# Performance work log

Measured on AMD Instinct MI355X. Metric: run time of the kernel, lower is better.

## Reference

```python
import jax, jax.numpy as jnp
import numpy as np

N_NODES = 100000
N_EDGES = 3200000
N_GRAPHS = 64


def _seg_mean(vals, idx, num_segments):
    s = jax.ops.segment_sum(vals, idx, num_segments=num_segments)
    cnt = jax.ops.segment_sum(jnp.ones((vals.shape[0],), vals.dtype), idx,
                              num_segments=num_segments)
    return s / jnp.maximum(cnt, 1.0)[:, None]


def _gcn_layer(x, edge_index, edge_attr, Wc, bc, Wn):
    # center = lin1(x)
    center = x @ Wc + bc
    row, col = edge_index[0], edge_index[1]  # row = source (j), col = target (i)
    # degree computed over row indices (as in PyG degree(row))
    deg = jax.ops.segment_sum(jnp.ones((row.shape[0],), x.dtype), row,
                              num_segments=x.shape[0])
    deg_inv_sqrt = jnp.where(deg > 0, jax.lax.rsqrt(jnp.maximum(deg, 1.0)), 0.0)
    norm = deg_inv_sqrt[row] * deg_inv_sqrt[col]  # [E]
    # message: lin2(concat(x_j, edge_attr)) * norm
    msg = jnp.concatenate([x[row], edge_attr], axis=1) @ Wn  # [E, out]
    msg = msg * norm[:, None]
    # aggr='mean' at target nodes
    aggr = _seg_mean(msg, col, x.shape[0])
    return center + aggr


def setup_inputs() -> dict:
    key = jax.random.key(0)
    ks = jax.random.split(key, 12)
    x = jax.random.normal(ks[0], (N_NODES, 3), dtype=jnp.float32)
    edge_index = jax.random.randint(ks[1], (2, N_EDGES), 0, N_NODES, dtype=jnp.int64)
    edge_attr = jax.random.normal(ks[2], (N_EDGES, 2), dtype=jnp.float32)
    batch = jnp.sort(jax.random.randint(ks[3], (N_NODES,), 0, N_GRAPHS, dtype=jnp.int64))
    s = 0.2
    params = {
        'Wc1': jax.random.normal(ks[4], (3, 16), jnp.float32) * s,
        'bc1': jnp.zeros((16,), jnp.float32),
        'Wn1': jax.random.normal(ks[5], (5, 16), jnp.float32) * s,   # in+edge = 3+2
        'Wc2': jax.random.normal(ks[6], (16, 16), jnp.float32) * s,
        'bc2': jnp.zeros((16,), jnp.float32),
        'Wn2': jax.random.normal(ks[7], (18, 16), jnp.float32) * s,  # 16+2
        'Wl1': jax.random.normal(ks[8], (16, 16), jnp.float32) * s,
        'bl1': jnp.zeros((16,), jnp.float32),
        'Wl2': jax.random.normal(ks[9], (16, 2), jnp.float32) * s,
        'bl2': jnp.zeros((2,), jnp.float32),
    }
    return dict(x=x, edge_index=edge_index, edge_attr=edge_attr, batch=batch, **params)


def reference(x, edge_index, edge_attr, batch,
              Wc1, bc1, Wn1, Wc2, bc2, Wn2, Wl1, bl1, Wl2, bl2):
    h = _gcn_layer(x, edge_index, edge_attr, Wc1, bc1, Wn1)
    h = jax.nn.relu(h)  # dropout is identity in eval mode
    h = _gcn_layer(h, edge_index, edge_attr, Wc2, bc2, Wn2)
    h = jax.nn.relu(h)
    g = _seg_mean(h, batch, N_GRAPHS)          # global scatter_mean pooling [G,16]
    g = jax.nn.relu(g @ Wl1 + bl1)
    return g @ Wl2 + bl2                        # [G, 2]
```

## Files before the change

kernel.cpp:

```cpp
#include <hip/hip_runtime.h>

constexpr int TPB  = 256;
constexpr int TPBW = 1024;
constexpr int TPBS = 512;
constexpr int BSH  = 7;
constexpr int BKN  = 128;
constexpr int MAXB = 800;
constexpr int CAP  = 4608;
constexpr int SBUF = 4608;
constexpr int ITER = 9;
constexpr int SIT  = 7;
constexpr int SEDG = SIT * TPBW;
constexpr int HWL  = 12800;

__device__ __forceinline__ unsigned short f2bf(float f) {
    unsigned u = __float_as_uint(f);
    u += 0x7FFFu + ((u >> 16) & 1u);
    return (unsigned short)(u >> 16);
}
__device__ __forceinline__ float bflo(unsigned u) {
    return __uint_as_float(u << 16);
}
__device__ __forceinline__ float bfhi(unsigned u) {
    return __uint_as_float(u & 0xFFFF0000u);
}

__global__ __launch_bounds__(TPBW)
void k_stage2(const int* __restrict__ ei, const float2* __restrict__ ea,
              int E, int NBKT, int W,
              int* __restrict__ gcnt, int2* __restrict__ staged,
              unsigned int* __restrict__ partialR) {
    __shared__ unsigned int lh[HWL];
    __shared__ int2 sb2[SEDG];
    __shared__ unsigned short sbk[SEDG];
    __shared__ int cl[MAXB], gb[MAXB], rs[MAXB + 1];
    __shared__ int tmp[1024];
    const int p = blockIdx.x, t = threadIdx.x;
    for (int i = t; i < W; i += TPBW) lh[i] = 0;
    for (int b = t; b < NBKT; b += TPBW) cl[b] = 0;
    __syncthreads();
    const int* colA = ei + E;
    const int s = p * SEDG, send = min(s + SEDG, E);
    int rid[SIT], eap[SIT], bk[SIT], rk[SIT];
#pragma unroll
    for (int k = 0; k < SIT; k++) {
        int e = s + t + k * TPBW;
        bk[k] = -1;
        if (e < send) {
            int r = ei[e], c = colA[e];
            atomicAdd(&lh[r >> 3], 1u << ((r & 7) * 4));
            int b = c >> BSH;
            float2 ev = ea[e];
            rid[k] = (r << BSH) | (c & (BKN - 1));
            eap[k] = (int)((unsigned)f2bf(ev.x) | ((unsigned)f2bf(ev.y) << 16));
            bk[k] = b;
            rk[k] = atomicAdd(&cl[b], 1);
        }
    }
    __syncthreads();
    tmp[t] = (t < NBKT) ? cl[t] : 0;
    __syncthreads();
    for (int off = 1; off < 1024; off <<= 1) {
        int add = (t >= off) ? tmp[t - off] : 0;
        __syncthreads();
        tmp[t] += add;
        __syncthreads();
    }
    if (t < NBKT) rs[t] = tmp[t] - cl[t];
    if (t == NBKT - 1) rs[NBKT] = tmp[t];
    __syncthreads();
    for (int b = t; b < NBKT; b += TPBW) {
        int c = cl[b];
        gb[b] = c ? atomicAdd(&gcnt[b], c) : 0;
    }
    __syncthreads();
#pragma unroll
    for (int k = 0; k < SIT; k++)
        if (bk[k] >= 0) {
            int slot = rs[bk[k]] + rk[k];
            sb2[slot] = make_int2(rid[k], eap[k]);
            sbk[slot] = (unsigned short)bk[k];
        }
    __syncthreads();
    const int total = rs[NBKT];
    for (int i = t; i < total; i += TPBW) {
        int b = sbk[i];
        int pos = gb[b] + (i - rs[b]);
        if (pos < CAP) staged[(size_t)b * CAP + pos] = sb2[i];
    }
    for (int w = t; w < W; w += TPBW) partialR[(size_t)p * W + w] = lh[w];
}

__global__ __launch_bounds__(512)
void k_xd(const unsigned int* __restrict__ partialR, int NP, int W, int N,
          const float* __restrict__ x,
          float* __restrict__ dis, float4* __restrict__ xd) {
    __shared__ unsigned int sA[8][64], sB[8][64];
    const int wloc = threadIdx.x & 63, lane = threadIdx.x >> 6;
    const int w = blockIdx.x * 64 + wloc;
    unsigned int accA = 0, accB = 0;
    if (w < W) {
        for (int p = lane; p < NP; p += 8) {
            unsigned int v = partialR[(size_t)p * W + w];
            accA += v & 0x0F0F0F0Fu;
            accB += (v >> 4) & 0x0F0F0F0Fu;
        }
    }
    sA[lane][wloc] = accA;
    sB[lane][wloc] = accB;
    __syncthreads();
    if (lane == 0 && w < W) {
#pragma unroll
        for (int l = 1; l < 8; l++) { accA += sA[l][wloc]; accB += sB[l][wloc]; }
        int d[8];
        d[0] = accA & 255; d[2] = (accA >> 8) & 255;
        d[4] = (accA >> 16) & 255; d[6] = accA >> 24;
        d[1] = accB & 255; d[3] = (accB >> 8) & 255;
        d[5] = (accB >> 16) & 255; d[7] = accB >> 24;
        const int n0 = w * 8;
#pragma unroll
        for (int k = 0; k < 8; k++) {
            int n = n0 + k;
            if (n < N) {
                float dv = d[k] ? rsqrtf((float)d[k]) : 0.f;
                dis[n] = dv;
                xd[n] = make_float4(x[3 * (size_t)n], x[3 * (size_t)n + 1],
                                    x[3 * (size_t)n + 2], dv);
            }
        }
    }
}

__global__ __launch_bounds__(TPBS)
void k_sortA(int2* __restrict__ staged, const int* __restrict__ gcnt,
             const float4* __restrict__ xd, int N,
             const float* __restrict__ Wc, const float* __restrict__ bc,
             const float* __restrict__ Wn,
             unsigned short* __restrict__ hb, unsigned short* __restrict__ hbs,
             float2* __restrict__ eaS,
             int* __restrict__ cnt, int* __restrict__ base, int* __restrict__ segN) {
    __shared__ int2 sbuf2[SBUF];
    __shared__ int lfill[BKN], lexc[BKN];
    __shared__ float sax[BKN], say[BKN], saz[BKN], se1[BKN], se2[BKN];
    __shared__ float sWc[48], sbc[16], sWn[80];
    __shared__ int stot;
    const int b = blockIdx.x, t = threadIdx.x;
    const size_t s0 = (size_t)b * CAP;
    const int c0 = b << BSH;
    int cb = gcnt[b]; if (cb > CAP) cb = CAP;
    if (t < BKN) lfill[t] = 0;
    if (t < 48) sWc[t] = Wc[t];
    if (t >= 64 && t < 80) sbc[t - 64] = bc[t - 64];
    if (t >= 128 && t < 208) sWn[t - 128] = Wn[t - 128];
    __syncthreads();
    int er[ITER], ep[ITER], rk[ITER];
#pragma unroll
    for (int k = 0; k < ITER; k++) {
        int e = t + k * TPBS;
        rk[k] = -1;
        if (e < cb) {
            int2 v = staged[s0 + e];
            int j = v.x & (BKN - 1);
            er[k] = (int)(((unsigned)v.x) >> BSH);
            ep[k] = v.y;
            rk[k] = atomicAdd(&lfill[j], 1) | (j << 16);
        }
    }
    __syncthreads();
    if (t < 64) {
        int v0 = lfill[2 * t], v1 = lfill[2 * t + 1];
        int sv = v0 + v1, incl = sv;
#pragma unroll
        for (int off = 1; off < 64; off <<= 1) {
            int up = __shfl_up(incl, off, 64);
            if (t >= off) incl += up;
        }
        int exc = incl - sv;
        lexc[2 * t]     = exc;
        lexc[2 * t + 1] = exc + v0;
        if (t == 63) stot = incl;
    }
    __syncthreads();
#pragma unroll
    for (int k = 0; k < ITER; k++) {
        if (rk[k] >= 0) {
            int j = rk[k] >> 16, rr = rk[k] & 0xFFFF;
            sbuf2[lexc[j] + rr] = make_int2(er[k], ep[k]);
        }
    }
    __syncthreads();
    int tot = stot; if (tot > SBUF) tot = SBUF;
    const int grp = t >> 2, sub = t & 3;
    const int node = c0 + grp;
    float a0 = 0.f, a1 = 0.f, a2 = 0.f, b1 = 0.f, b2 = 0.f;
    {
        int e0 = lexc[grp], dg = lfill[grp];
        if (node < N) {
            for (int e = sub; e < dg; e += 8) {
                int2 ve0 = sbuf2[e0 + e];
                bool v1 = (e + 4) < dg;
                int2 ve1 = v1 ? sbuf2[e0 + e + 4] : ve0;
                float4 q0 = xd[ve0.x];
                float4 q1 = xd[ve1.x];
                float w0 = q0.w;
                float w1 = v1 ? q1.w : 0.f;
                a0 += w0 * q0.x + w1 * q1.x;
                a1 += w0 * q0.y + w1 * q1.y;
                a2 += w0 * q0.z + w1 * q1.z;
                b1 += w0 * bflo((unsigned)ve0.y) + w1 * bflo((unsigned)ve1.y);
                b2 += w0 * bfhi((unsigned)ve0.y) + w1 * bfhi((unsigned)ve1.y);
            }
        }
    }
    a0 += __shfl_down(a0, 2, 4); a0 += __shfl_down(a0, 1, 4);
    a1 += __shfl_down(a1, 2, 4); a1 += __shfl_down(a1, 1, 4);
    a2 += __shfl_down(a2, 2, 4); a2 += __shfl_down(a2, 1, 4);
    b1 += __shfl_down(b1, 2, 4); b1 += __shfl_down(b1, 1, 4);
    b2 += __shfl_down(b2, 2, 4); b2 += __shfl_down(b2, 1, 4);
    if (sub == 0) {
        sax[grp] = a0; say[grp] = a1; saz[grp] = a2;
        se1[grp] = b1; se2[grp] = b2;
    }
    {
        int* ridS = (int*)staged;
        for (int i = t; i < tot; i += TPBS) ridS[s0 * 2 + i] = sbuf2[i].x;
    }
    if (t == 0) segN[b] = tot;
    if (t < BKN) {
        int nd = c0 + t;
        if (nd < N) { cnt[nd] = lfill[t]; base[nd] = lexc[t]; }
    }
    __syncthreads();
    if (t < BKN) {
        int nd = c0 + t;
        if (nd < N) {
            float inv = 1.0f / fmaxf((float)lfill[t], 1.0f);
            float4 xq = xd[nd];
            float ldt = xq.w;
            float sc = ldt * inv;
            float m[5] = {sax[t] * sc, say[t] * sc, saz[t] * sc,
                          se1[t] * sc, se2[t] * sc};
            float xv[3] = {xq.x, xq.y, xq.z};
            float o[16];
#pragma unroll
            for (int k = 0; k < 16; k++) {
                float v = sbc[k];
#pragma unroll
                for (int j = 0; j < 3; j++) v += xv[j] * sWc[j * 16 + k];
#pragma unroll
                for (int j = 0; j < 5; j++) v += m[j] * sWn[j * 16 + k];
                o[k] = fmaxf(v, 0.0f);
            }
            unsigned ov[8], sv[8];
#pragma unroll
            for (int q = 0; q < 8; q++) {
                ov[q] = (unsigned)f2bf(o[2 * q]) | ((unsigned)f2bf(o[2 * q + 1]) << 16);
                sv[q] = (unsigned)f2bf(ldt * o[2 * q]) |
                        ((unsigned)f2bf(ldt * o[2 * q + 1]) << 16);
            }
            uint4* hp = (uint4*)(hb + 16 * (size_t)nd);
            hp[0] = make_uint4(ov[0], ov[1], ov[2], ov[3]);
            hp[1] = make_uint4(ov[4], ov[5], ov[6], ov[7]);
            uint4* hps = (uint4*)(hbs + 16 * (size_t)nd);
            hps[0] = make_uint4(sv[0], sv[1], sv[2], sv[3]);
            hps[1] = make_uint4(sv[4], sv[5], sv[6], sv[7]);
            eaS[nd] = make_float2(se1[t] * ldt, se2[t] * ldt);
        }
    }
}

__global__ __launch_bounds__(TPBS)
void k_g2(const int* __restrict__ ridS, const int* __restrict__ cnt,
          const int* __restrict__ base, const int* __restrict__ segN,
          const float* __restrict__ dis, const unsigned short* __restrict__ hb,
          const unsigned short* __restrict__ hbs,
          const float2* __restrict__ eaS, const int* __restrict__ batch, int N,
          const float* __restrict__ Wc, const float* __restrict__ bc,
          const float* __restrict__ Wn,
          float* __restrict__ pool, int* __restrict__ poolcnt) {
    __shared__ int sbuf[SBUF];
    __shared__ int lfill[BKN], lexc[BKN];
    __shared__ float smr[BKN][17];
    __shared__ float sWc[256], sbc[16], sWn[288], sp[1024];
    __shared__ int sc[64];
    const int b = blockIdx.x, t = threadIdx.x;
    const size_t s0 = (size_t)b * CAP * 2;
    const int c0 = b << BSH;
    if (t < BKN) {
        int nd = c0 + t;
        lfill[t] = (nd < N) ? cnt[nd] : 0;
        lexc[t]  = (nd < N) ? base[nd] : 0;
    }
    for (int k = t; k < 256; k += TPBS) sWc[k] = Wc[k];
    for (int k = t; k < 16;  k += TPBS) sbc[k] = bc[k];
    for (int k = t; k < 288; k += TPBS) sWn[k] = Wn[k];
    for (int k = t; k < 1024; k += TPBS) sp[k] = 0.f;
    if (t < 64) sc[t] = 0;
    int tot = segN[b];
    if (tot > SBUF) tot = SBUF;
    for (int i = t; i < tot; i += TPBS) sbuf[i] = ridS[s0 + i];
    __syncthreads();
    const int grp = t >> 2, sub = t & 3;
    const int node = c0 + grp;
    float mm[16];
#pragma unroll
    for (int k = 0; k < 16; k++) mm[k] = 0.f;
    if (node < N) {
        int e0 = lexc[grp], dg = lfill[grp];
        for (int e = sub; e < dg; e += 8) {
            int r0 = sbuf[e0 + e];
            bool v1 = (e + 4) < dg;
            int r1 = v1 ? sbuf[e0 + e + 4] : r0;
            const uint4* h0 = (const uint4*)(hbs + 16 * (size_t)r0);
            const uint4* h1 = (const uint4*)(hbs + 16 * (size_t)r1);
            uint4 A0 = h0[0], B0 = h0[1];
            uint4 A1 = h1[0], B1 = h1[1];
            float s1 = v1 ? 1.f : 0.f;
            mm[0]  += bflo(A0.x) + s1 * bflo(A1.x);
            mm[1]  += bfhi(A0.x) + s1 * bfhi(A1.x);
            mm[2]  += bflo(A0.y) + s1 * bflo(A1.y);
            mm[3]  += bfhi(A0.y) + s1 * bfhi(A1.y);
            mm[4]  += bflo(A0.z) + s1 * bflo(A1.z);
            mm[5]  += bfhi(A0.z) + s1 * bfhi(A1.z);
            mm[6]  += bflo(A0.w) + s1 * bflo(A1.w);
            mm[7]  += bfhi(A0.w) + s1 * bfhi(A1.w);
            mm[8]  += bflo(B0.x) + s1 * bflo(B1.x);
            mm[9]  += bfhi(B0.x) + s1 * bfhi(B1.x);
            mm[10] += bflo(B0.y) + s1 * bflo(B1.y);
            mm[11] += bfhi(B0.y) + s1 * bfhi(B1.y);
            mm[12] += bflo(B0.z) + s1 * bflo(B1.z);
            mm[13] += bfhi(B0.z) + s1 * bfhi(B1.z);
            mm[14] += bflo(B0.w) + s1 * bflo(B1.w);
            mm[15] += bfhi(B0.w) + s1 * bfhi(B1.w);
        }
    }
#pragma unroll
    for (int k = 0; k < 16; k++) {
        mm[k] += __shfl_down(mm[k], 2, 4);
        mm[k] += __shfl_down(mm[k], 1, 4);
    }
    if (sub == 0) {
#pragma unroll
        for (int k = 0; k < 16; k++) smr[grp][k] = mm[k];
    }
    __syncthreads();
    if (t < BKN) {
        int nd = c0 + t;
        if (nd < N) {
            float inv = 1.0f / fmaxf((float)lfill[t], 1.0f);
            float ldt = dis[nd];
            float scm = ldt * inv;
            float m[18];
#pragma unroll
            for (int k = 0; k < 16; k++) m[k] = smr[t][k] * scm;
            float2 es = eaS[nd];
            m[16] = es.x * inv; m[17] = es.y * inv;
            const uint4* hp = (const uint4*)(hb + 16 * (size_t)nd);
            uint4 A = hp[0], B = hp[1];
            float hv[16] = {bflo(A.x), bfhi(A.x), bflo(A.y), bfhi(A.y),
                            bflo(A.z), bfhi(A.z), bflo(A.w), bfhi(A.w),
                            bflo(B.x), bfhi(B.x), bflo(B.y), bfhi(B.y),
                            bflo(B.z), bfhi(B.z), bflo(B.w), bfhi(B.w)};
            int g = batch[nd];
            atomicAdd(&sc[g], 1);
#pragma unroll
            for (int k = 0; k < 16; k++) {
                float v = sbc[k];
#pragma unroll
                for (int j = 0; j < 16; j++) v += hv[j] * sWc[j * 16 + k];
#pragma unroll
                for (int j = 0; j < 18; j++) v += m[j] * sWn[j * 16 + k];
                v = fmaxf(v, 0.0f);
                unsafeAtomicAdd(&sp[g * 16 + k], v);
            }
        }
    }
    __syncthreads();
    for (int k = t; k < 1024; k += TPBS)
        if (sp[k] != 0.0f) unsafeAtomicAdd(&pool[k], sp[k]);
    if (t < 64 && sc[t]) atomicAdd(&poolcnt[t], sc[t]);
}

__global__ void k_final(const float* __restrict__ pool, const int* __restrict__ poolcnt,
                        const float* __restrict__ Wl1, const float* __restrict__ bl1,
                        const float* __restrict__ Wl2, const float* __restrict__ bl2,
                        float* __restrict__ out) {
    int g = threadIdx.x;
    if (g >= 64) return;
    float inv = 1.0f / fmaxf((float)poolcnt[g], 1.0f);
    float gv[16];
#pragma unroll
    for (int k = 0; k < 16; k++) gv[k] = pool[g * 16 + k] * inv;
    float t[16];
#pragma unroll
    for (int k = 0; k < 16; k++) {
        float v = bl1[k];
#pragma unroll
        for (int j = 0; j < 16; j++) v += gv[j] * Wl1[j * 16 + k];
        t[k] = fmaxf(v, 0.0f);
    }
    float o0 = bl2[0], o1 = bl2[1];
#pragma unroll
    for (int j = 0; j < 16; j++) {
        o0 += t[j] * Wl2[j * 2 + 0];
        o1 += t[j] * Wl2[j * 2 + 1];
    }
    out[2 * g + 0] = o0;
    out[2 * g + 1] = o1;
}

extern "C" void kernel_launch(void* const* d_in, const int* in_sizes, int n_in,
                              void* d_out, int out_size, void* d_ws, size_t ws_size,
                              hipStream_t stream) {
    const float* x     = (const float*)d_in[0];
    const int*   ei    = (const int*)  d_in[1];
    const float* ea    = (const float*)d_in[2];
    const int*   batch = (const int*)  d_in[3];
    const float* Wc1   = (const float*)d_in[4];
    const float* bc1   = (const float*)d_in[5];
    const float* Wn1   = (const float*)d_in[6];
    const float* Wc2   = (const float*)d_in[7];
    const float* bc2   = (const float*)d_in[8];
    const float* Wn2   = (const float*)d_in[9];
    const float* Wl1   = (const float*)d_in[10];
    const float* bl1   = (const float*)d_in[11];
    const float* Wl2   = (const float*)d_in[12];
    const float* bl2   = (const float*)d_in[13];
    float* out = (float*)d_out;

    const int N  = in_sizes[0] / 3;
    const int E  = in_sizes[1] / 2;
    const int NBKT = (N + BKN - 1) >> BSH;
    const int SGRID = (E + SEDG - 1) / SEDG;
    const int W = (N + 7) >> 3;

    char* ws = (char*)d_ws;
    size_t o = 0;
    auto alloc = [&](size_t bytes) {
        void* p = ws + o;
        o += (bytes + 255) & ~(size_t)255;
        return p;
    };
    float* pool    = (float*)alloc(64 * 16 * 4);
    int*   poolcnt = (int*)  alloc(64 * 4);
    int*   gcnt    = (int*)  alloc((size_t)NBKT * 4);
    size_t zbytes = o;
    float*  dis     = (float*)alloc((size_t)N * 4);
    float4* xd      = (float4*)alloc((size_t)N * 16);
    float2* eaS     = (float2*)alloc((size_t)N * 8);
    int*    cnt     = (int*)  alloc((size_t)N * 4);
    int*    base    = (int*)  alloc((size_t)N * 4);
    int*    segN    = (int*)  alloc((size_t)NBKT * 4);
    unsigned int* partialR = (unsigned int*)alloc((size_t)SGRID * W * 4);
    int2*   staged  = (int2*)alloc((size_t)NBKT * CAP * 8);
    unsigned short* hb  = (unsigned short*)alloc((size_t)N * 16 * 2);
    unsigned short* hbs = (unsigned short*)alloc((size_t)N * 16 * 2);
    (void)ws_size;

    hipMemsetAsync(d_ws, 0, zbytes, stream);

    k_stage2<<<SGRID, TPBW, 0, stream>>>(ei, (const float2*)ea, E, NBKT, W,
                                         gcnt, staged, partialR);
    k_xd    <<<(W + 63) / 64, 512, 0, stream>>>(partialR, SGRID, W, N, x, dis, xd);
    k_sortA <<<NBKT, TPBS, 0, stream>>>(staged, gcnt, xd, N,
                                        Wc1, bc1, Wn1, hb, hbs, eaS,
                                        cnt, base, segN);
    k_g2    <<<NBKT, TPBS, 0, stream>>>((const int*)staged, cnt, base, segN,
                                        dis, hb, hbs, eaS, batch, N,
                                        Wc2, bc2, Wn2, pool, poolcnt);
    k_final <<<1, 64, 0, stream>>>(pool, poolcnt, Wl1, bl1, Wl2, bl2, out);
}
```

Before: 237.6 us.

## Fuse degree, layer1, layer2 and head into one cooperative persistent kernel

```diff
diff --git a/kernel.cpp b/kernel.cpp
--- a/kernel.cpp
+++ b/kernel.cpp
@@ -1,13 +1,14 @@
 #include <hip/hip_runtime.h>
-
-constexpr int TPB  = 256;
+#include <hip/hip_cooperative_groups.h>
+
+namespace cg = cooperative_groups;
+
 constexpr int TPBW = 1024;
 constexpr int TPBS = 512;
 constexpr int BSH  = 7;
 constexpr int BKN  = 128;
 constexpr int MAXB = 800;
-constexpr int CAP  = 4608;
-constexpr int SBUF = 4608;
+constexpr int CAP  = 4544;
 constexpr int ITER = 9;
 constexpr int SIT  = 7;
 constexpr int SEDG = SIT * TPBW;
@@ -91,322 +92,369 @@
     for (int w = t; w < W; w += TPBW) partialR[(size_t)p * W + w] = lh[w];
 }
 
-__global__ __launch_bounds__(512)
-void k_xd(const unsigned int* __restrict__ partialR, int NP, int W, int N,
-          const float* __restrict__ x,
-          float* __restrict__ dis, float4* __restrict__ xd) {
-    __shared__ unsigned int sA[8][64], sB[8][64];
-    const int wloc = threadIdx.x & 63, lane = threadIdx.x >> 6;
-    const int w = blockIdx.x * 64 + wloc;
-    unsigned int accA = 0, accB = 0;
-    if (w < W) {
-        for (int p = lane; p < NP; p += 8) {
-            unsigned int v = partialR[(size_t)p * W + w];
-            accA += v & 0x0F0F0F0Fu;
-            accB += (v >> 4) & 0x0F0F0F0Fu;
-        }
-    }
-    sA[lane][wloc] = accA;
-    sB[lane][wloc] = accB;
-    __syncthreads();
-    if (lane == 0 && w < W) {
-#pragma unroll
-        for (int l = 1; l < 8; l++) { accA += sA[l][wloc]; accB += sB[l][wloc]; }
-        int d[8];
-        d[0] = accA & 255; d[2] = (accA >> 8) & 255;
-        d[4] = (accA >> 16) & 255; d[6] = accA >> 24;
-        d[1] = accB & 255; d[3] = (accB >> 8) & 255;
-        d[5] = (accB >> 16) & 255; d[7] = accB >> 24;
-        const int n0 = w * 8;
-#pragma unroll
-        for (int k = 0; k < 8; k++) {
-            int n = n0 + k;
-            if (n < N) {
-                float dv = d[k] ? rsqrtf((float)d[k]) : 0.f;
-                dis[n] = dv;
-                xd[n] = make_float4(x[3 * (size_t)n], x[3 * (size_t)n + 1],
-                                    x[3 * (size_t)n + 2], dv);
-            }
-        }
-    }
-}
-
 __global__ __launch_bounds__(TPBS)
-void k_sortA(int2* __restrict__ staged, const int* __restrict__ gcnt,
-             const float4* __restrict__ xd, int N,
-             const float* __restrict__ Wc, const float* __restrict__ bc,
-             const float* __restrict__ Wn,
+void k_fused(int2* __restrict__ staged, const int* __restrict__ gcnt,
+             const unsigned int* __restrict__ partialR, int NP, int W, int N,
+             const float* __restrict__ x, float* __restrict__ dis,
+             float4* __restrict__ xd,
+             const float* __restrict__ Wc1, const float* __restrict__ bc1,
+             const float* __restrict__ Wn1,
              unsigned short* __restrict__ hb, unsigned short* __restrict__ hbs,
              float2* __restrict__ eaS,
-             int* __restrict__ cnt, int* __restrict__ base, int* __restrict__ segN) {
-    __shared__ int2 sbuf2[SBUF];
+             int* __restrict__ cnt, int* __restrict__ base, int* __restrict__ segN,
+             const int* __restrict__ batch,
+             const float* __restrict__ Wc2, const float* __restrict__ bc2,
+             const float* __restrict__ Wn2,
+             float* __restrict__ pool, int* __restrict__ poolcnt,
+             const float* __restrict__ Wl1, const float* __restrict__ bl1,
+             const float* __restrict__ Wl2, const float* __restrict__ bl2,
+             float* __restrict__ out, int NBKT) {
+    cg::grid_group grid = cg::this_grid();
+    __shared__ int2 sbuf2[CAP];
     __shared__ int lfill[BKN], lexc[BKN];
-    __shared__ float sax[BKN], say[BKN], saz[BKN], se1[BKN], se2[BKN];
-    __shared__ float sWc[48], sbc[16], sWn[80];
-    __shared__ int stot;
-    const int b = blockIdx.x, t = threadIdx.x;
-    const size_t s0 = (size_t)b * CAP;
-    const int c0 = b << BSH;
-    int cb = gcnt[b]; if (cb > CAP) cb = CAP;
-    if (t < BKN) lfill[t] = 0;
-    if (t < 48) sWc[t] = Wc[t];
-    if (t >= 64 && t < 80) sbc[t - 64] = bc[t - 64];
-    if (t >= 128 && t < 208) sWn[t - 128] = Wn[t - 128];
-    __syncthreads();
-    int er[ITER], ep[ITER], rk[ITER];
-#pragma unroll
-    for (int k = 0; k < ITER; k++) {
-        int e = t + k * TPBS;
-        rk[k] = -1;
-        if (e < cb) {
-            int2 v = staged[s0 + e];
-            int j = v.x & (BKN - 1);
-            er[k] = (int)(((unsigned)v.x) >> BSH);
-            ep[k] = v.y;
-            rk[k] = atomicAdd(&lfill[j], 1) | (j << 16);
-        }
-    }
-    __syncthreads();
-    if (t < 64) {
-        int v0 = lfill[2 * t], v1 = lfill[2 * t + 1];
-        int sv = v0 + v1, incl = sv;
-#pragma unroll
-        for (int off = 1; off < 64; off <<= 1) {
-            int up = __shfl_up(incl, off, 64);
-            if (t >= off) incl += up;
-        }
-        int exc = incl - sv;
-        lexc[2 * t]     = exc;
-        lexc[2 * t + 1] = exc + v0;
-        if (t == 63) stot = incl;
-    }
-    __syncthreads();
-#pragma unroll
-    for (int k = 0; k < ITER; k++) {
-        if (rk[k] >= 0) {
-            int j = rk[k] >> 16, rr = rk[k] & 0xFFFF;
-            sbuf2[lexc[j] + rr] = make_int2(er[k], ep[k]);
-        }
-    }
-    __syncthreads();
-    int tot = stot; if (tot > SBUF) tot = SBUF;
-    const int grp = t >> 2, sub = t & 3;
-    const int node = c0 + grp;
-    float a0 = 0.f, a1 = 0.f, a2 = 0.f, b1 = 0.f, b2 = 0.f;
+    __shared__ float facc[5][BKN];
+    __shared__ float sw1[144];
+    __shared__ int stot, keepTot;
+    int* ibuf = (int*)sbuf2;
+    const int t = threadIdx.x;
+
     {
-        int e0 = lexc[grp], dg = lfill[grp];
-        if (node < N) {
-            for (int e = sub; e < dg; e += 8) {
-                int2 ve0 = sbuf2[e0 + e];
-                bool v1 = (e + 4) < dg;
-                int2 ve1 = v1 ? sbuf2[e0 + e + 4] : ve0;
-                float4 q0 = xd[ve0.x];
-                float4 q1 = xd[ve1.x];
-                float w0 = q0.w;
-                float w1 = v1 ? q1.w : 0.f;
-                a0 += w0 * q0.x + w1 * q1.x;
-                a1 += w0 * q0.y + w1 * q1.y;
-                a2 += w0 * q0.z + w1 * q1.z;
-                b1 += w0 * bflo((unsigned)ve0.y) + w1 * bflo((unsigned)ve1.y);
-                b2 += w0 * bfhi((unsigned)ve0.y) + w1 * bfhi((unsigned)ve1.y);
-            }
-        }
-    }
-    a0 += __shfl_down(a0, 2, 4); a0 += __shfl_down(a0, 1, 4);
-    a1 += __shfl_down(a1, 2, 4); a1 += __shfl_down(a1, 1, 4);
-    a2 += __shfl_down(a2, 2, 4); a2 += __shfl_down(a2, 1, 4);
-    b1 += __shfl_down(b1, 2, 4); b1 += __shfl_down(b1, 1, 4);
-    b2 += __shfl_down(b2, 2, 4); b2 += __shfl_down(b2, 1, 4);
-    if (sub == 0) {
-        sax[grp] = a0; say[grp] = a1; saz[grp] = a2;
-        se1[grp] = b1; se2[grp] = b2;
-    }
-    {
-        int* ridS = (int*)staged;
-        for (int i = t; i < tot; i += TPBS) ridS[s0 * 2 + i] = sbuf2[i].x;
-    }
-    if (t == 0) segN[b] = tot;
-    if (t < BKN) {
-        int nd = c0 + t;
-        if (nd < N) { cnt[nd] = lfill[t]; base[nd] = lexc[t]; }
-    }
-    __syncthreads();
-    if (t < BKN) {
-        int nd = c0 + t;
-        if (nd < N) {
-            float inv = 1.0f / fmaxf((float)lfill[t], 1.0f);
-            float4 xq = xd[nd];
-            float ldt = xq.w;
-            float sc = ldt * inv;
-            float m[5] = {sax[t] * sc, say[t] * sc, saz[t] * sc,
-                          se1[t] * sc, se2[t] * sc};
-            float xv[3] = {xq.x, xq.y, xq.z};
-            float o[16];
+        const int nxb = (W + 63) >> 6;
+        if ((int)blockIdx.x < nxb) {
+            unsigned int* sA = (unsigned int*)ibuf;
+            unsigned int* sB = sA + 512;
+            const int wloc = t & 63, lane = t >> 6;
+            const int w = blockIdx.x * 64 + wloc;
+            unsigned int accA = 0, accB = 0;
+            if (w < W) {
+                for (int p = lane; p < NP; p += 8) {
+                    unsigned int v = partialR[(size_t)p * W + w];
+                    accA += v & 0x0F0F0F0Fu;
+                    accB += (v >> 4) & 0x0F0F0F0Fu;
+                }
+            }
+            sA[lane * 64 + wloc] = accA;
+            sB[lane * 64 + wloc] = accB;
+            __syncthreads();
+            if (lane == 0 && w < W) {
+#pragma unroll
+                for (int l = 1; l < 8; l++) {
+                    accA += sA[l * 64 + wloc];
+                    accB += sB[l * 64 + wloc];
+                }
+                int d[8];
+                d[0] = accA & 255; d[2] = (accA >> 8) & 255;
+                d[4] = (accA >> 16) & 255; d[6] = accA >> 24;
+                d[1] = accB & 255; d[3] = (accB >> 8) & 255;
+                d[5] = (accB >> 16) & 255; d[7] = accB >> 24;
+                const int n0 = w * 8;
+#pragma unroll
+                for (int k = 0; k < 8; k++) {
+                    int n = n0 + k;
+                    if (n < N) {
+                        float dv = d[k] ? rsqrtf((float)d[k]) : 0.f;
+                        dis[n] = dv;
+                        xd[n] = make_float4(x[3 * (size_t)n], x[3 * (size_t)n + 1],
+                                            x[3 * (size_t)n + 2], dv);
+                    }
+                }
+            }
+        }
+    }
+    __threadfence();
+    grid.sync();
+
+    if (t < 48) sw1[t] = Wc1[t];
+    else if (t < 64) sw1[t] = bc1[t - 48];
+    else if (t < 144) sw1[t] = Wn1[t - 64];
+
+    int own[4], nb = 0;
+    for (int b = blockIdx.x; b < NBKT && nb < 4; b += (int)gridDim.x) own[nb++] = b;
+
+    for (int q = 0; q < nb; q++) {
+        const int b = own[q];
+        const size_t s0 = (size_t)b * CAP;
+        const int c0 = b << BSH;
+        int cb = gcnt[b]; if (cb > CAP) cb = CAP;
+        __syncthreads();
+        if (t < BKN) {
+            lfill[t] = 0;
+            facc[0][t] = 0.f; facc[1][t] = 0.f; facc[2][t] = 0.f;
+            facc[3][t] = 0.f; facc[4][t] = 0.f;
+        }
+        __syncthreads();
+        int er[ITER], ep[ITER], rk[ITER];
+#pragma unroll
+        for (int k = 0; k < ITER; k++) {
+            int e = t + k * TPBS;
+            rk[k] = -1;
+            if (e < cb) {
+                int2 v = staged[s0 + e];
+                int j = v.x & (BKN - 1);
+                er[k] = (int)(((unsigned)v.x) >> BSH);
+                ep[k] = v.y;
+                rk[k] = atomicAdd(&lfill[j], 1) | (j << 16);
+            }
+        }
+        __syncthreads();
+        if (t < 64) {
+            int v0 = lfill[2 * t], v1 = lfill[2 * t + 1];
+            int sv = v0 + v1, incl = sv;
+#pragma unroll
+            for (int off = 1; off < 64; off <<= 1) {
+                int up = __shfl_up(incl, off, 64);
+                if (t >= off) incl += up;
+            }
+            int exc = incl - sv;
+            lexc[2 * t] = exc;
+            lexc[2 * t + 1] = exc + v0;
+            if (t == 63) stot = incl;
+        }
+        __syncthreads();
+#pragma unroll
+        for (int k = 0; k < ITER; k++) {
+            if (rk[k] >= 0) {
+                int j = rk[k] >> 16, rr = rk[k] & 0xFFFF;
+                sbuf2[lexc[j] + rr] = make_int2(er[k], ep[k]);
+            }
+        }
+        __syncthreads();
+        int tot = stot; if (tot > CAP) tot = CAP;
+        {
+            const int grp = t >> 2, sub = t & 3;
+            const int node = c0 + grp;
+            float a0 = 0.f, a1 = 0.f, a2 = 0.f, e1 = 0.f, e2 = 0.f;
+            int e0 = lexc[grp], dg = lfill[grp];
+            if (node < N) {
+                for (int e = sub; e < dg; e += 8) {
+                    int2 ve0 = sbuf2[e0 + e];
+                    bool ok1 = (e + 4) < dg;
+                    int2 ve1 = ok1 ? sbuf2[e0 + e + 4] : ve0;
+                    float4 q0 = xd[ve0.x];
+                    float4 q1 = xd[ve1.x];
+                    float w0 = q0.w;
+                    float w1v = ok1 ? q1.w : 0.f;
+                    a0 += w0 * q0.x + w1v * q1.x;
+                    a1 += w0 * q0.y + w1v * q1.y;
+                    a2 += w0 * q0.z + w1v * q1.z;
+                    e1 += w0 * bflo((unsigned)ve0.y) + w1v * bflo((unsigned)ve1.y);
+                    e2 += w0 * bfhi((unsigned)ve0.y) + w1v * bfhi((unsigned)ve1.y);
+                }
+            }
+            a0 += __shfl_down(a0, 2, 4); a0 += __shfl_down(a0, 1, 4);
+            a1 += __shfl_down(a1, 2, 4); a1 += __shfl_down(a1, 1, 4);
+            a2 += __shfl_down(a2, 2, 4); a2 += __shfl_down(a2, 1, 4);
+            e1 += __shfl_down(e1, 2, 4); e1 += __shfl_down(e1, 1, 4);
+            e2 += __shfl_down(e2, 2, 4); e2 += __shfl_down(e2, 1, 4);
+            if (sub == 0) {
+                facc[0][grp] = a0; facc[1][grp] = a1; facc[2][grp] = a2;
+                facc[3][grp] = e1; facc[4][grp] = e2;
+            }
+        }
+        if (t == 0) segN[b] = tot;
+        if (t < BKN) {
+            int nd = c0 + t;
+            if (nd < N) { cnt[nd] = lfill[t]; base[nd] = lexc[t]; }
+        }
+        __syncthreads();
+        if (q == nb - 1) {
+            int rv[ITER];
+#pragma unroll
+            for (int k = 0; k < ITER; k++) {
+                int i = t + k * TPBS;
+                rv[k] = (i < tot) ? sbuf2[i].x : 0;
+            }
+            __syncthreads();
+#pragma unroll
+            for (int k = 0; k < ITER; k++) {
+                int i = t + k * TPBS;
+                if (i < tot) ibuf[i] = rv[k];
+            }
+            if (t == 0) keepTot = tot;
+        } else {
+            int* ridS = (int*)staged;
+            for (int i = t; i < tot; i += TPBS) ridS[s0 * 2 + i] = sbuf2[i].x;
+        }
+        __syncthreads();
+        if (t < BKN) {
+            int nd = c0 + t;
+            if (nd < N) {
+                float inv = 1.0f / fmaxf((float)lfill[t], 1.0f);
+                float4 xq = xd[nd];
+                float ldt = xq.w;
+                float sc = ldt * inv;
+                float m[5] = {facc[0][t] * sc, facc[1][t] * sc, facc[2][t] * sc,
+                              facc[3][t] * sc, facc[4][t] * sc};
+                float xv[3] = {xq.x, xq.y, xq.z};
+                float o[16];
+#pragma unroll
+                for (int k = 0; k < 16; k++) {
+                    float v = sw1[48 + k];
+#pragma unroll
+                    for (int j = 0; j < 3; j++) v += xv[j] * sw1[j * 16 + k];
+#pragma unroll
+                    for (int j = 0; j < 5; j++) v += m[j] * sw1[64 + j * 16 + k];
+                    o[k] = fmaxf(v, 0.0f);
+                }
+                unsigned ov[8], sv[8];
+#pragma unroll
+                for (int p2 = 0; p2 < 8; p2++) {
+                    ov[p2] = (unsigned)f2bf(o[2 * p2]) |
+                             ((unsigned)f2bf(o[2 * p2 + 1]) << 16);
+                    sv[p2] = (unsigned)f2bf(ldt * o[2 * p2]) |
+                             ((unsigned)f2bf(ldt * o[2 * p2 + 1]) << 16);
+                }
+                uint4* hp = (uint4*)(hb + 16 * (size_t)nd);
+                hp[0] = make_uint4(ov[0], ov[1], ov[2], ov[3]);
+                hp[1] = make_uint4(ov[4], ov[5], ov[6], ov[7]);
+                uint4* hps = (uint4*)(hbs + 16 * (size_t)nd);
+                hps[0] = make_uint4(sv[0], sv[1], sv[2], sv[3]);
+                hps[1] = make_uint4(sv[4], sv[5], sv[6], sv[7]);
+                eaS[nd] = make_float2(facc[3][t] * ldt, facc[4][t] * ldt);
+            }
+        }
+    }
+    __threadfence();
+    grid.sync();
+
+    float* smr = (float*)(ibuf + 4608);
+    float* spl = (float*)(ibuf + 6784);
+    float* sW2 = (float*)(ibuf + 7808);
+    float* sN2 = (float*)(ibuf + 8064);
+    float* sB2 = (float*)(ibuf + 8352);
+    int*   scc = ibuf + 8368;
+    for (int k = t; k < 256; k += TPBS) sW2[k] = Wc2[k];
+    for (int k = t; k < 288; k += TPBS) sN2[k] = Wn2[k];
+    if (t < 16) sB2[t] = bc2[t];
+    for (int k = t; k < 1024; k += TPBS) spl[k] = 0.f;
+    if (t < 64) scc[t] = 0;
+    for (int q = nb - 1; q >= 0; q--) {
+        const int b = own[q];
+        const bool res = (q == nb - 1);
+        const int c0 = b << BSH;
+        __syncthreads();
+        int tot;
+        if (res) {
+            tot = keepTot;
+        } else {
+            tot = segN[b]; if (tot > CAP) tot = CAP;
+            const int* ridS = (const int*)staged;
+            for (int i = t; i < tot; i += TPBS) ibuf[i] = ridS[(size_t)b * CAP * 2 + i];
+            if (t < BKN) {
+                int nd = c0 + t;
+                lfill[t] = (nd < N) ? cnt[nd] : 0;
+                lexc[t]  = (nd < N) ? base[nd] : 0;
+            }
+        }
+        __syncthreads();
+        {
+            const int grp = t >> 2, sub = t & 3;
+            const int node = c0 + grp;
+            float mm[16];
+#pragma unroll
+            for (int k = 0; k < 16; k++) mm[k] = 0.f;
+            if (node < N) {
+                int e0 = lexc[grp], dg = lfill[grp];
+                for (int e = sub; e < dg; e += 8) {
+                    int r0 = ibuf[e0 + e];
+                    bool ok1 = (e + 4) < dg;
+                    int r1 = ok1 ? ibuf[e0 + e + 4] : r0;
+                    const uint4* h0 = (const uint4*)(hbs + 16 * (size_t)r0);
+                    const uint4* h1 = (const uint4*)(hbs + 16 * (size_t)r1);
+                    uint4 A0 = h0[0], B0 = h0[1];
+                    uint4 A1 = h1[0], B1 = h1[1];
+                    float s1 = ok1 ? 1.f : 0.f;
+                    mm[0]  += bflo(A0.x) + s1 * bflo(A1.x);
+                    mm[1]  += bfhi(A0.x) + s1 * bfhi(A1.x);
+                    mm[2]  += bflo(A0.y) + s1 * bflo(A1.y);
+                    mm[3]  += bfhi(A0.y) + s1 * bfhi(A1.y);
+                    mm[4]  += bflo(A0.z) + s1 * bflo(A1.z);
+                    mm[5]  += bfhi(A0.z) + s1 * bfhi(A1.z);
+                    mm[6]  += bflo(A0.w) + s1 * bflo(A1.w);
+                    mm[7]  += bfhi(A0.w) + s1 * bfhi(A1.w);
+                    mm[8]  += bflo(B0.x) + s1 * bflo(B1.x);
+                    mm[9]  += bfhi(B0.x) + s1 * bfhi(B1.x);
+                    mm[10] += bflo(B0.y) + s1 * bflo(B1.y);
+                    mm[11] += bfhi(B0.y) + s1 * bfhi(B1.y);
+                    mm[12] += bflo(B0.z) + s1 * bflo(B1.z);
+                    mm[13] += bfhi(B0.z) + s1 * bfhi(B1.z);
+                    mm[14] += bflo(B0.w) + s1 * bflo(B1.w);
+                    mm[15] += bfhi(B0.w) + s1 * bfhi(B1.w);
+                }
+            }
 #pragma unroll
             for (int k = 0; k < 16; k++) {
-                float v = sbc[k];
-#pragma unroll
-                for (int j = 0; j < 3; j++) v += xv[j] * sWc[j * 16 + k];
-#pragma unroll
-                for (int j = 0; j < 5; j++) v += m[j] * sWn[j * 16 + k];
-                o[k] = fmaxf(v, 0.0f);
-            }
-            unsigned ov[8], sv[8];
-#pragma unroll
-            for (int q = 0; q < 8; q++) {
-                ov[q] = (unsigned)f2bf(o[2 * q]) | ((unsigned)f2bf(o[2 * q + 1]) << 16);
-                sv[q] = (unsigned)f2bf(ldt * o[2 * q]) |
-                        ((unsigned)f2bf(ldt * o[2 * q + 1]) << 16);
-            }
-            uint4* hp = (uint4*)(hb + 16 * (size_t)nd);
-            hp[0] = make_uint4(ov[0], ov[1], ov[2], ov[3]);
-            hp[1] = make_uint4(ov[4], ov[5], ov[6], ov[7]);
-            uint4* hps = (uint4*)(hbs + 16 * (size_t)nd);
-            hps[0] = make_uint4(sv[0], sv[1], sv[2], sv[3]);
-            hps[1] = make_uint4(sv[4], sv[5], sv[6], sv[7]);
-            eaS[nd] = make_float2(se1[t] * ldt, se2[t] * ldt);
-        }
-    }
-}
-
-__global__ __launch_bounds__(TPBS)
-void k_g2(const int* __restrict__ ridS, const int* __restrict__ cnt,
-          const int* __restrict__ base, const int* __restrict__ segN,
-          const float* __restrict__ dis, const unsigned short* __restrict__ hb,
-          const unsigned short* __restrict__ hbs,
-          const float2* __restrict__ eaS, const int* __restrict__ batch, int N,
-          const float* __restrict__ Wc, const float* __restrict__ bc,
-          const float* __restrict__ Wn,
-          float* __restrict__ pool, int* __restrict__ poolcnt) {
-    __shared__ int sbuf[SBUF];
-    __shared__ int lfill[BKN], lexc[BKN];
-    __shared__ float smr[BKN][17];
-    __shared__ float sWc[256], sbc[16], sWn[288], sp[1024];
-    __shared__ int sc[64];
-    const int b = blockIdx.x, t = threadIdx.x;
-    const size_t s0 = (size_t)b * CAP * 2;
-    const int c0 = b << BSH;
-    if (t < BKN) {
-        int nd = c0 + t;
-        lfill[t] = (nd < N) ? cnt[nd] : 0;
-        lexc[t]  = (nd < N) ? base[nd] : 0;
-    }
-    for (int k = t; k < 256; k += TPBS) sWc[k] = Wc[k];
-    for (int k = t; k < 16;  k += TPBS) sbc[k] = bc[k];
-    for (int k = t; k < 288; k += TPBS) sWn[k] = Wn[k];
-    for (int k = t; k < 1024; k += TPBS) sp[k] = 0.f;
-    if (t < 64) sc[t] = 0;
-    int tot = segN[b];
-    if (tot > SBUF) tot = SBUF;
-    for (int i = t; i < tot; i += TPBS) sbuf[i] = ridS[s0 + i];
-    __syncthreads();
-    const int grp = t >> 2, sub = t & 3;
-    const int node = c0 + grp;
-    float mm[16];
-#pragma unroll
-    for (int k = 0; k < 16; k++) mm[k] = 0.f;
-    if (node < N) {
-        int e0 = lexc[grp], dg = lfill[grp];
-        for (int e = sub; e < dg; e += 8) {
-            int r0 = sbuf[e0 + e];
-            bool v1 = (e + 4) < dg;
-            int r1 = v1 ? sbuf[e0 + e + 4] : r0;
-            const uint4* h0 = (const uint4*)(hbs + 16 * (size_t)r0);
-            const uint4* h1 = (const uint4*)(hbs + 16 * (size_t)r1);
-            uint4 A0 = h0[0], B0 = h0[1];
-            uint4 A1 = h1[0], B1 = h1[1];
-            float s1 = v1 ? 1.f : 0.f;
-            mm[0]  += bflo(A0.x) + s1 * bflo(A1.x);
-            mm[1]  += bfhi(A0.x) + s1 * bfhi(A1.x);
-            mm[2]  += bflo(A0.y) + s1 * bflo(A1.y);
-            mm[3]  += bfhi(A0.y) + s1 * bfhi(A1.y);
-            mm[4]  += bflo(A0.z) + s1 * bflo(A1.z);
-            mm[5]  += bfhi(A0.z) + s1 * bfhi(A1.z);
-            mm[6]  += bflo(A0.w) + s1 * bflo(A1.w);
-            mm[7]  += bfhi(A0.w) + s1 * bfhi(A1.w);
-            mm[8]  += bflo(B0.x) + s1 * bflo(B1.x);
-            mm[9]  += bfhi(B0.x) + s1 * bfhi(B1.x);
-            mm[10] += bflo(B0.y) + s1 * bflo(B1.y);
-            mm[11] += bfhi(B0.y) + s1 * bfhi(B1.y);
-            mm[12] += bflo(B0.z) + s1 * bflo(B1.z);
-            mm[13] += bfhi(B0.z) + s1 * bfhi(B1.z);
-            mm[14] += bflo(B0.w) + s1 * bflo(B1.w);
-            mm[15] += bfhi(B0.w) + s1 * bfhi(B1.w);
-        }
-    }
-#pragma unroll
-    for (int k = 0; k < 16; k++) {
-        mm[k] += __shfl_down(mm[k], 2, 4);
-        mm[k] += __shfl_down(mm[k], 1, 4);
-    }
-    if (sub == 0) {
-#pragma unroll
-        for (int k = 0; k < 16; k++) smr[grp][k] = mm[k];
-    }
-    __syncthreads();
-    if (t < BKN) {
-        int nd = c0 + t;
-        if (nd < N) {
-            float inv = 1.0f / fmaxf((float)lfill[t], 1.0f);
-            float ldt = dis[nd];
-            float scm = ldt * inv;
-            float m[18];
-#pragma unroll
-            for (int k = 0; k < 16; k++) m[k] = smr[t][k] * scm;
-            float2 es = eaS[nd];
-            m[16] = es.x * inv; m[17] = es.y * inv;
-            const uint4* hp = (const uint4*)(hb + 16 * (size_t)nd);
-            uint4 A = hp[0], B = hp[1];
-            float hv[16] = {bflo(A.x), bfhi(A.x), bflo(A.y), bfhi(A.y),
-                            bflo(A.z), bfhi(A.z), bflo(A.w), bfhi(A.w),
-                            bflo(B.x), bfhi(B.x), bflo(B.y), bfhi(B.y),
-                            bflo(B.z), bfhi(B.z), bflo(B.w), bfhi(B.w)};
-            int g = batch[nd];
-            atomicAdd(&sc[g], 1);
-#pragma unroll
-            for (int k = 0; k < 16; k++) {
-                float v = sbc[k];
-#pragma unroll
-                for (int j = 0; j < 16; j++) v += hv[j] * sWc[j * 16 + k];
-#pragma unroll
-                for (int j = 0; j < 18; j++) v += m[j] * sWn[j * 16 + k];
-                v = fmaxf(v, 0.0f);
-                unsafeAtomicAdd(&sp[g * 16 + k], v);
+                mm[k] += __shfl_down(mm[k], 2, 4);
+                mm[k] += __shfl_down(mm[k], 1, 4);
+            }
+            if (sub == 0) {
+#pragma unroll
+                for (int k = 0; k < 16; k++) smr[grp * 17 + k] = mm[k];
+            }
+        }
+        __syncthreads();
+        if (t < BKN) {
+            int nd = c0 + t;
+            if (nd < N) {
+                float inv = 1.0f / fmaxf((float)lfill[t], 1.0f);
+                float ldt = dis[nd];
+                float scm = ldt * inv;
+                float m[18];
+#pragma unroll
+                for (int k = 0; k < 16; k++) m[k] = smr[t * 17 + k] * scm;
+                float2 es = eaS[nd];
+                m[16] = es.x * inv; m[17] = es.y * inv;
+                const uint4* hp = (const uint4*)(hb + 16 * (size_t)nd);
+                uint4 A = hp[0], B = hp[1];
+                float hv[16] = {bflo(A.x), bfhi(A.x), bflo(A.y), bfhi(A.y),
+                                bflo(A.z), bfhi(A.z), bflo(A.w), bfhi(A.w),
+                                bflo(B.x), bfhi(B.x), bflo(B.y), bfhi(B.y),
+                                bflo(B.z), bfhi(B.z), bflo(B.w), bfhi(B.w)};
+                int g = batch[nd];
+                atomicAdd(&scc[g], 1);
+#pragma unroll
+                for (int k = 0; k < 16; k++) {
+                    float v = sB2[k];
+#pragma unroll
+                    for (int j = 0; j < 16; j++) v += hv[j] * sW2[j * 16 + k];
+#pragma unroll
+                    for (int j = 0; j < 18; j++) v += m[j] * sN2[j * 16 + k];
+                    v = fmaxf(v, 0.0f);
+                    unsafeAtomicAdd(&spl[g * 16 + k], v);
+                }
             }
         }
     }
     __syncthreads();
     for (int k = t; k < 1024; k += TPBS)
-        if (sp[k] != 0.0f) unsafeAtomicAdd(&pool[k], sp[k]);
-    if (t < 64 && sc[t]) atomicAdd(&poolcnt[t], sc[t]);
-}
-
-__global__ void k_final(const float* __restrict__ pool, const int* __restrict__ poolcnt,
-                        const float* __restrict__ Wl1, const float* __restrict__ bl1,
-                        const float* __restrict__ Wl2, const float* __restrict__ bl2,
-                        float* __restrict__ out) {
-    int g = threadIdx.x;
-    if (g >= 64) return;
-    float inv = 1.0f / fmaxf((float)poolcnt[g], 1.0f);
-    float gv[16];
-#pragma unroll
-    for (int k = 0; k < 16; k++) gv[k] = pool[g * 16 + k] * inv;
-    float t[16];
-#pragma unroll
-    for (int k = 0; k < 16; k++) {
-        float v = bl1[k];
-#pragma unroll
-        for (int j = 0; j < 16; j++) v += gv[j] * Wl1[j * 16 + k];
-        t[k] = fmaxf(v, 0.0f);
-    }
-    float o0 = bl2[0], o1 = bl2[1];
-#pragma unroll
-    for (int j = 0; j < 16; j++) {
-        o0 += t[j] * Wl2[j * 2 + 0];
-        o1 += t[j] * Wl2[j * 2 + 1];
-    }
-    out[2 * g + 0] = o0;
-    out[2 * g + 1] = o1;
+        if (spl[k] != 0.0f) unsafeAtomicAdd(&pool[k], spl[k]);
+    if (t < 64 && scc[t]) atomicAdd(&poolcnt[t], scc[t]);
+    __threadfence();
+    grid.sync();
+
+    if (blockIdx.x == 0 && t < 64) {
+        int g = t;
+        float inv = 1.0f / fmaxf((float)poolcnt[g], 1.0f);
+        float gv[16];
+#pragma unroll
+        for (int k = 0; k < 16; k++) gv[k] = pool[g * 16 + k] * inv;
+        float tt[16];
+#pragma unroll
+        for (int k = 0; k < 16; k++) {
+            float v = bl1[k];
+#pragma unroll
+            for (int j = 0; j < 16; j++) v += gv[j] * Wl1[j * 16 + k];
+            tt[k] = fmaxf(v, 0.0f);
+        }
+        float o0 = bl2[0], o1 = bl2[1];
+#pragma unroll
+        for (int j = 0; j < 16; j++) {
+            o0 += tt[j] * Wl2[j * 2 + 0];
+            o1 += tt[j] * Wl2[j * 2 + 1];
+        }
+        out[2 * g + 0] = o0;
+        out[2 * g + 1] = o1;
+    }
 }
 
 extern "C" void kernel_launch(void* const* d_in, const int* in_sizes, int n_in,
@@ -461,12 +509,24 @@
 
     k_stage2<<<SGRID, TPBW, 0, stream>>>(ei, (const float2*)ea, E, NBKT, W,
                                          gcnt, staged, partialR);
-    k_xd    <<<(W + 63) / 64, 512, 0, stream>>>(partialR, SGRID, W, N, x, dis, xd);
-    k_sortA <<<NBKT, TPBS, 0, stream>>>(staged, gcnt, xd, N,
-                                        Wc1, bc1, Wn1, hb, hbs, eaS,
-                                        cnt, base, segN);
-    k_g2    <<<NBKT, TPBS, 0, stream>>>((const int*)staged, cnt, base, segN,
-                                        dis, hb, hbs, eaS, batch, N,
-                                        Wc2, bc2, Wn2, pool, poolcnt);
-    k_final <<<1, 64, 0, stream>>>(pool, poolcnt, Wl1, bl1, Wl2, bl2, out);
+
+    int maxb = 0;
+    hipOccupancyMaxActiveBlocksPerMultiprocessor(&maxb, k_fused, TPBS, 0);
+    if (maxb < 1) maxb = 1;
+    int GRIDF = maxb * 256;
+    if (GRIDF > NBKT) GRIDF = NBKT;
+
+    int NPv = SGRID, Wv = W, Nv = N, NBKTv = NBKT;
+    void* kargs[] = {
+        (void*)&staged, (void*)&gcnt, (void*)&partialR, (void*)&NPv, (void*)&Wv,
+        (void*)&Nv, (void*)&x, (void*)&dis, (void*)&xd,
+        (void*)&Wc1, (void*)&bc1, (void*)&Wn1,
+        (void*)&hb, (void*)&hbs, (void*)&eaS,
+        (void*)&cnt, (void*)&base, (void*)&segN,
+        (void*)&batch, (void*)&Wc2, (void*)&bc2, (void*)&Wn2,
+        (void*)&pool, (void*)&poolcnt,
+        (void*)&Wl1, (void*)&bl1, (void*)&Wl2, (void*)&bl2,
+        (void*)&out, (void*)&NBKTv
+    };
+    hipLaunchCooperativeKernel(k_fused, dim3(GRIDF), dim3(TPBS), kargs, 0, stream);
 }
```

Result: slower. 499.6 us (+110.2%).
